# Performance work log

Hardware: AMD Instinct MI355X
Metric: run time of the kernel (lower is better)

The kernel has to match this reference:

```python
import jax, jax.numpy as jnp
import numpy as np

NEG_SLOPE = 0.01  # torch LeakyReLU default

def _rgcn_layer(x, comp_l, basis_l, root_l, bias_l, src, dst, etype, n_nodes):
    # basis decomposition: per-relation weight [R, in, out]
    w = jnp.einsum('rb,bio->rio', comp_l, basis_l)
    # transform every node by every relation: [N, R, out]
    xw = jnp.einsum('ni,rio->nro', x, w)
    # per-edge message = transformed source feature for the edge's relation
    m = xw[src, etype]                                  # [E, out]
    agg = jax.ops.segment_sum(m, dst, num_segments=n_nodes)  # scatter-add
    return agg + x @ root_l + bias_l

def setup_inputs() -> dict:
    key = jax.random.key(0)
    ks = jax.random.split(key, 12)
    N, E, R, B, D, L = 50000, 1600000, 8, 4, 240, 2
    s = 1.0 / np.sqrt(D)
    return {
        'x': jax.random.normal(ks[0], (N, D), jnp.float32),
        'edge_index': jax.random.randint(ks[1], (2, E), 0, N, jnp.int64),
        'edge_type': jax.random.randint(ks[2], (E,), 0, R, jnp.int64),
        'comp': jax.random.normal(ks[3], (L, R, B), jnp.float32) * 0.5,
        'basis': jax.random.normal(ks[4], (L, B, D, D), jnp.float32) * s,
        'root': jax.random.normal(ks[5], (L, D, D), jnp.float32) * s,
        'bias': jax.random.normal(ks[6], (L, D), jnp.float32) * 0.01,
        'W1': jax.random.normal(ks[7], (128, 2 * D), jnp.float32) / np.sqrt(2 * D),
        'b1': jax.random.normal(ks[8], (128,), jnp.float32) * 0.01,
        'W2': jax.random.normal(ks[9], (1, 128), jnp.float32) / np.sqrt(128),
        'b2': jax.random.normal(ks[10], (1,), jnp.float32) * 0.01,
        'concept_index': 0,
        'sentence_index': 1,
    }

def reference(x, edge_index, edge_type, comp, basis, root, bias, W1, b1, W2, b2,
              concept_index, sentence_index):
    n_nodes = x.shape[0]
    num_layers = comp.shape[0]
    src, dst = edge_index[0], edge_index[1]
    h = x
    for i in range(num_layers):
        h = _rgcn_layer(h, comp[i], basis[i], root[i], bias[i], src, dst, edge_type, n_nodes)
        if i != num_layers - 1:
            h = jax.nn.leaky_relu(h, NEG_SLOPE)  # dropout is identity at inference
    h_s = h[sentence_index]
    h_c = h[concept_index]
    h_cat = jnp.concatenate([jnp.abs(h_s - h_c), h_s * h_c], axis=-1)  # [2D]
    hidden = jax.nn.leaky_relu(h_cat @ W1.T + b1, NEG_SLOPE)
    out = hidden @ W2.T + b2  # [1]
    return out
```

## Files before the change

### kernel.cpp

```cpp
#include <hip/hip_runtime.h>
#include <cstdint>
#include <cstddef>

#define N_NODES 50000
#define N_EDGES 1600000
#define N_REL 8
#define N_BASIS 4
#define DIM 240
#define NEG_SLOPE 0.01f

#define CAP_S1 256
#define CAP_DEG 128
#define BITMAP_WORDS ((N_NODES + 31) / 32)
#define NCH 8
#define CHUNK (DIM / NCH)

__device__ __forceinline__ float lrelu(float v) { return v > 0.f ? v : NEG_SLOPE * v; }

__global__ __launch_bounds__(256) void k_pass1(const int* __restrict__ ei,
                                               const int* __restrict__ cip,
                                               const int* __restrict__ sip,
                                               unsigned* __restrict__ bitmap) {
    int base = (blockIdx.x * 256 + threadIdx.x) * 4;
    int ci = cip[0], si = sip[0];
    if (blockIdx.x == 0 && threadIdx.x == 0) {
        atomicOr(&bitmap[ci >> 5], 1u << (ci & 31));
        atomicOr(&bitmap[si >> 5], 1u << (si & 31));
    }
    if (base < N_EDGES) {
        int4 d = *reinterpret_cast<const int4*>(ei + N_EDGES + base);
        int dv[4] = {d.x, d.y, d.z, d.w};
#pragma unroll
        for (int j = 0; j < 4; j++) {
            if (dv[j] == ci || dv[j] == si) {
                int src = ei[base + j];
                atomicOr(&bitmap[src >> 5], 1u << (src & 31));
            }
        }
    }
}

__global__ __launch_bounds__(256) void k_compact(const unsigned* __restrict__ bitmap,
                                                 int* __restrict__ map,
                                                 int* __restrict__ nodes,
                                                 int* __restrict__ cnts) {
    int n = blockIdx.x * 256 + threadIdx.x;
    if (n < N_NODES && ((bitmap[n >> 5] >> (n & 31)) & 1u)) {
        int slot = atomicAdd(&cnts[0], 1);
        if (slot < CAP_S1) {
            map[n] = slot;
            nodes[slot] = n;
        } else {
            map[n] = -1;
        }
    }
}

__global__ __launch_bounds__(256) void k_pass2(const int* __restrict__ ei,
                                               const int* __restrict__ et,
                                               const unsigned* __restrict__ bitmap,
                                               const int* __restrict__ map,
                                               int* __restrict__ degs,
                                               unsigned* __restrict__ eslot) {
    int base = (blockIdx.x * 256 + threadIdx.x) * 4;
    if (base < N_EDGES) {
        int4 d = *reinterpret_cast<const int4*>(ei + N_EDGES + base);
        int dv[4] = {d.x, d.y, d.z, d.w};
#pragma unroll
        for (int j = 0; j < 4; j++) {
            int dst = dv[j];
            if ((bitmap[dst >> 5] >> (dst & 31)) & 1u) {
                int slot = map[dst];
                if (slot >= 0) {
                    int idx = atomicAdd(&degs[slot], 1);
                    if (idx < CAP_DEG) {
                        unsigned src = (unsigned)ei[base + j];
                        unsigned ty  = (unsigned)et[base + j];
                        eslot[(size_t)slot * CAP_DEG + idx] = src | (ty << 16);
                    }
                }
            }
        }
    }
}

__global__ __launch_bounds__(256) void k_z1(const float* __restrict__ x,
                                            const unsigned* __restrict__ eslot,
                                            const int* __restrict__ degs,
                                            const int* __restrict__ nodes,
                                            const int* __restrict__ cnts,
                                            const float* __restrict__ compL,
                                            float* __restrict__ z1) {
    int slot = blockIdx.x;
    if (slot >= min(cnts[0], CAP_S1)) return;
    int t = threadIdx.x;
    __shared__ unsigned els[CAP_DEG];
    __shared__ float cs[N_REL * N_BASIS];
    int deg = min(degs[slot], CAP_DEG);
    if (t < N_REL * N_BASIS) cs[t] = compL[t];
    if (t < deg) els[t] = eslot[(size_t)slot * CAP_DEG + t];
    __syncthreads();
    if (t < DIM) {
        float z0 = 0.f, z1a = 0.f, z2a = 0.f, z3a = 0.f;
        int base = 0;
        for (; base + 4 <= deg; base += 4) {
            float xv[4];
            int ty[4];
#pragma unroll
            for (int j = 0; j < 4; j++) {
                unsigned p = els[base + j];
                int src = (int)(p & 0xFFFFu);
                ty[j] = (int)(p >> 16);
                xv[j] = x[(size_t)src * DIM + t];
            }
#pragma unroll
            for (int j = 0; j < 4; j++) {
                const float* c = &cs[ty[j] * N_BASIS];
                z0 += c[0] * xv[j]; z1a += c[1] * xv[j];
                z2a += c[2] * xv[j]; z3a += c[3] * xv[j];
            }
        }
        for (; base < deg; base++) {
            unsigned p = els[base];
            int src = (int)(p & 0xFFFFu);
            const float* c = &cs[(p >> 16) * N_BASIS];
            float xv = x[(size_t)src * DIM + t];
            z0 += c[0] * xv; z1a += c[1] * xv; z2a += c[2] * xv; z3a += c[3] * xv;
        }
        int node = nodes[slot];
        float xn = x[(size_t)node * DIM + t];
        float* zp = z1 + (size_t)slot * 5 * DIM;
        zp[0 * DIM + t] = z0;  zp[1 * DIM + t] = z1a;
        zp[2 * DIM + t] = z2a; zp[3 * DIM + t] = z3a;
        zp[4 * DIM + t] = xn;
    }
}

__global__ __launch_bounds__(256) void k_hgemm(const float* __restrict__ z1,
                                               const int* __restrict__ cnts,
                                               const float* __restrict__ basisL,
                                               const float* __restrict__ rootL,
                                               float* __restrict__ h1raw) {
    int slot = blockIdx.x;
    if (slot >= min(cnts[0], CAP_S1)) return;
    int ch = blockIdx.y;
    int i0 = ch * CHUNK;
    int t = threadIdx.x;
    __shared__ float zc[5][CHUNK];
    if (t < 5 * CHUNK) {
        int b = t / CHUNK, ii = t % CHUNK;
        zc[b][ii] = z1[((size_t)slot * 5 + b) * DIM + i0 + ii];
    }
    __syncthreads();
    if (t < DIM) {
        float acc = 0.f;
#pragma unroll 5
        for (int ii = 0; ii < CHUNK; ii++) {
            int i = i0 + ii;
            acc += zc[0][ii] * basisL[(size_t)(0 * DIM + i) * DIM + t];
            acc += zc[1][ii] * basisL[(size_t)(1 * DIM + i) * DIM + t];
            acc += zc[2][ii] * basisL[(size_t)(2 * DIM + i) * DIM + t];
            acc += zc[3][ii] * basisL[(size_t)(3 * DIM + i) * DIM + t];
            acc += zc[4][ii] * rootL[(size_t)i * DIM + t];
        }
        atomicAdd(&h1raw[(size_t)slot * DIM + t], acc);
    }
}

__global__ __launch_bounds__(256) void k_zh2(const float* __restrict__ h1raw,
                                             const unsigned* __restrict__ eslot,
                                             const int* __restrict__ degs,
                                             const int* __restrict__ map,
                                             const float* __restrict__ comp2,
                                             const float* __restrict__ bias1,
                                             const float* __restrict__ basis2,
                                             const float* __restrict__ root2,
                                             const int* __restrict__ cip,
                                             const int* __restrict__ sip,
                                             float* __restrict__ h2acc) {
    int w = blockIdx.x, ch = blockIdx.y;
    int i0 = ch * CHUNK;
    int t = threadIdx.x;
    __shared__ unsigned els[CAP_DEG];
    __shared__ float cs[N_REL * N_BASIS];
    __shared__ float zpart[8][N_BASIS][CHUNK];
    __shared__ float zc[5][CHUNK];
    int node = w ? sip[0] : cip[0];
    int slot = map[node];
    int deg = (slot >= 0) ? min(degs[slot], CAP_DEG) : 0;
    if (t < N_REL * N_BASIS) cs[t] = comp2[t];
    if (t < deg) els[t] = eslot[(size_t)slot * CAP_DEG + t];
    __syncthreads();
    if (t < 8 * CHUNK) {
        int e8 = t / CHUNK, d = t % CHUNK;
        float za0 = 0.f, za1 = 0.f, za2 = 0.f, za3 = 0.f;
        for (int base = 0; base < deg; base += 8) {
            int e = base + e8;
            if (e < deg) {
                unsigned p = els[e];
                int src = (int)(p & 0xFFFFu);
                int ty  = (int)(p >> 16);
                int ss = map[src];
                float hv = 0.f;
                if (ss >= 0)
                    hv = lrelu(h1raw[(size_t)ss * DIM + i0 + d] + bias1[i0 + d]);
                const float* c = &cs[ty * N_BASIS];
                za0 += c[0] * hv; za1 += c[1] * hv; za2 += c[2] * hv; za3 += c[3] * hv;
            }
        }
        zpart[e8][0][d] = za0; zpart[e8][1][d] = za1;
        zpart[e8][2][d] = za2; zpart[e8][3][d] = za3;
    }
    __syncthreads();
    if (t < N_BASIS * CHUNK) {
        int b = t / CHUNK, d = t % CHUNK;
        float s = 0.f;
#pragma unroll
        for (int e = 0; e < 8; e++) s += zpart[e][b][d];
        zc[b][d] = s;
    } else if (t >= N_BASIS * CHUNK && t < 5 * CHUNK) {
        int d = t - N_BASIS * CHUNK;
        float r = (slot >= 0) ? lrelu(h1raw[(size_t)slot * DIM + i0 + d] + bias1[i0 + d]) : 0.f;
        zc[4][d] = r;
    }
    __syncthreads();
    if (t < DIM) {
        float acc = 0.f;
#pragma unroll 5
        for (int ii = 0; ii < CHUNK; ii++) {
            int i = i0 + ii;
            acc += zc[0][ii] * basis2[(size_t)(0 * DIM + i) * DIM + t];
            acc += zc[1][ii] * basis2[(size_t)(1 * DIM + i) * DIM + t];
            acc += zc[2][ii] * basis2[(size_t)(2 * DIM + i) * DIM + t];
            acc += zc[3][ii] * basis2[(size_t)(3 * DIM + i) * DIM + t];
            acc += zc[4][ii] * root2[(size_t)i * DIM + t];
        }
        atomicAdd(&h2acc[w * DIM + t], acc);
    }
}

__global__ __launch_bounds__(512) void k_head(const float* __restrict__ h2acc,
                                              const float* __restrict__ bias2,
                                              const float* __restrict__ W1,
                                              const float* __restrict__ b1,
                                              const float* __restrict__ W2,
                                              const float* __restrict__ b2,
                                              float* __restrict__ out) {
    __shared__ float cat[2 * DIM];
    __shared__ float part[128][4];
    __shared__ float hid[128];
    int t = threadIdx.x;
    if (t < DIM) {
        float hc = h2acc[t] + bias2[t];
        float hs = h2acc[DIM + t] + bias2[t];
        cat[t] = fabsf(hs - hc);
        cat[DIM + t] = hs * hc;
    }
    __syncthreads();
    int r = t >> 2, q = t & 3;
    const float4* wr = reinterpret_cast<const float4*>(W1 + (size_t)r * 2 * DIM) + q * 30;
    const float4* cq = reinterpret_cast<const float4*>(cat) + q * 30;
    float acc = 0.f;
#pragma unroll 6
    for (int k = 0; k < 30; k++) {
        float4 wv = wr[k];
        float4 cv = cq[k];
        acc += wv.x * cv.x + wv.y * cv.y + wv.z * cv.z + wv.w * cv.w;
    }
    part[r][q] = acc;
    __syncthreads();
    if (q == 0) {
        float s = part[r][0] + part[r][1] + part[r][2] + part[r][3] + b1[r];
        hid[r] = lrelu(s) * W2[r];
    }
    __syncthreads();
    if (t < 64) {
        float v = hid[t] + hid[t + 64];
        for (int off = 32; off > 0; off >>= 1) v += __shfl_down(v, off);
        if (t == 0) out[0] = b2[0] + v;
    }
}

extern "C" void kernel_launch(void* const* d_in, const int* in_sizes, int n_in,
                              void* d_out, int out_size, void* d_ws, size_t ws_size,
                              hipStream_t stream) {
    const float* x     = (const float*)d_in[0];
    const int*   ei    = (const int*)d_in[1];
    const int*   et    = (const int*)d_in[2];
    const float* comp  = (const float*)d_in[3];
    const float* basis = (const float*)d_in[4];
    const float* root  = (const float*)d_in[5];
    const float* bias  = (const float*)d_in[6];
    const float* W1    = (const float*)d_in[7];
    const float* b1    = (const float*)d_in[8];
    const float* W2    = (const float*)d_in[9];
    const float* b2    = (const float*)d_in[10];
    const int*   cip   = (const int*)d_in[11];
    const int*   sip   = (const int*)d_in[12];
    float* out = (float*)d_out;
    (void)n_in; (void)in_sizes; (void)out_size;

    char* ws = (char*)d_ws;
    size_t off = 0;
    auto alloc = [&](size_t bytes) -> char* {
        char* p = ws + off;
        off += (bytes + 255) & ~(size_t)255;
        return p;
    };
    size_t zbeg = off;
    int*      cnts   = (int*)alloc(2 * sizeof(int));
    int*      degs   = (int*)alloc((size_t)CAP_S1 * sizeof(int));
    unsigned* bitmap = (unsigned*)alloc(BITMAP_WORDS * sizeof(unsigned));
    float*    h2acc  = (float*)alloc((size_t)2 * DIM * sizeof(float));
    float*    h1raw  = (float*)alloc((size_t)CAP_S1 * DIM * sizeof(float));
    size_t zend = off;
    int*      map    = (int*)alloc((size_t)N_NODES * sizeof(int));
    int*      nodes  = (int*)alloc((size_t)CAP_S1 * sizeof(int));
    unsigned* eslot  = (unsigned*)alloc((size_t)CAP_S1 * CAP_DEG * sizeof(unsigned));
    float*    z1     = (float*)alloc((size_t)CAP_S1 * 5 * DIM * sizeof(float));
    if (off > ws_size) return;

    hipMemsetAsync(ws + zbeg, 0, zend - zbeg, stream);

    const float* comp2  = comp  + N_REL * N_BASIS;
    const float* basis2 = basis + (size_t)N_BASIS * DIM * DIM;
    const float* root2  = root  + (size_t)DIM * DIM;
    const float* bias2  = bias  + DIM;

    int egrid4 = (N_EDGES / 4 + 255) / 256;
    k_pass1<<<egrid4, 256, 0, stream>>>(ei, cip, sip, bitmap);
    k_compact<<<(N_NODES + 255) / 256, 256, 0, stream>>>(bitmap, map, nodes, cnts);
    k_pass2<<<egrid4, 256, 0, stream>>>(ei, et, bitmap, map, degs, eslot);

    k_z1<<<CAP_S1, 256, 0, stream>>>(x, eslot, degs, nodes, cnts, comp, z1);
    k_hgemm<<<dim3(CAP_S1, NCH), 256, 0, stream>>>(z1, cnts, basis, root, h1raw);
    k_zh2<<<dim3(2, NCH), 256, 0, stream>>>(h1raw, eslot, degs, map, comp2, bias,
                                            basis2, root2, cip, sip, h2acc);
    k_head<<<1, 512, 0, stream>>>(h2acc, bias2, W1, b1, W2, b2, out);
}
```

Measured before the change: 170.9 us.

## Fuse RGCN pipeline stages and drop bitmap/compact pass and memset

Replaces the bitmap, compact pass and memset with an init kernel plus atomicCAS claiming of node slots directly in the map. It fuses the per-node basis aggregation with the dense basis/root GEMM, recomputing the aggregation per output chunk instead of writing z1 and atomically adding partial results. The layer-2 stage and the MLP head are merged into one kernel, where the last block to finish (tracked by a completion counter) runs the head. This cuts the number of kernel launches and intermediate global traffic, at the cost of redundant gathers of x across the eight chunk blocks.

```diff
diff --git a/kernel.cpp b/kernel.cpp
--- a/kernel.cpp
+++ b/kernel.cpp
@@ -11,272 +11,265 @@
 
 #define CAP_S1 256
 #define CAP_DEG 128
-#define BITMAP_WORDS ((N_NODES + 31) / 32)
 #define NCH 8
 #define CHUNK (DIM / NCH)
 
+#define WS_CNT    0
+#define WS_DONE   8
+#define WS_DEGS   256
+#define WS_MAP    1280
+#define WS_NODES  201344
+#define WS_ESLOT  202496
+#define WS_H1C    333568
+#define WS_H2     579328
+#define WS_TOTAL  581248
+
 __device__ __forceinline__ float lrelu(float v) { return v > 0.f ? v : NEG_SLOPE * v; }
 
-__global__ __launch_bounds__(256) void k_pass1(const int* __restrict__ ei,
-                                               const int* __restrict__ cip,
-                                               const int* __restrict__ sip,
-                                               unsigned* __restrict__ bitmap) {
+__global__ __launch_bounds__(256) void k_init(int* __restrict__ cnt,
+                                              int* __restrict__ done,
+                                              int* __restrict__ degs,
+                                              int* __restrict__ map) {
+    int t = blockIdx.x * 256 + threadIdx.x;
+    int nth = gridDim.x * 256;
+    for (int n = t; n < N_NODES; n += nth) map[n] = -1;
+    for (int i = t; i < CAP_S1; i += nth) degs[i] = 0;
+    if (t == 0) { cnt[0] = 0; done[0] = 0; }
+}
+
+__device__ __forceinline__ void claim_node(int n, int* map, int* nodes, int* cnt) {
+    int old = atomicCAS(&map[n], -1, -2);
+    if (old == -1) {
+        int s = atomicAdd(cnt, 1);
+        if (s < CAP_S1) { nodes[s] = n; map[n] = s; }
+        else map[n] = -1;
+    }
+}
+
+__global__ __launch_bounds__(256) void k_mark(const int* __restrict__ ei,
+                                              const int* __restrict__ cip,
+                                              const int* __restrict__ sip,
+                                              int* __restrict__ map,
+                                              int* __restrict__ nodes,
+                                              int* __restrict__ cnt) {
     int base = (blockIdx.x * 256 + threadIdx.x) * 4;
     int ci = cip[0], si = sip[0];
-    if (blockIdx.x == 0 && threadIdx.x == 0) {
-        atomicOr(&bitmap[ci >> 5], 1u << (ci & 31));
-        atomicOr(&bitmap[si >> 5], 1u << (si & 31));
-    }
+    if (blockIdx.x == 0 && threadIdx.x < 2)
+        claim_node(threadIdx.x ? si : ci, map, nodes, cnt);
     if (base < N_EDGES) {
         int4 d = *reinterpret_cast<const int4*>(ei + N_EDGES + base);
         int dv[4] = {d.x, d.y, d.z, d.w};
 #pragma unroll
-        for (int j = 0; j < 4; j++) {
-            if (dv[j] == ci || dv[j] == si) {
-                int src = ei[base + j];
-                atomicOr(&bitmap[src >> 5], 1u << (src & 31));
-            }
-        }
-    }
-}
-
-__global__ __launch_bounds__(256) void k_compact(const unsigned* __restrict__ bitmap,
-                                                 int* __restrict__ map,
-                                                 int* __restrict__ nodes,
-                                                 int* __restrict__ cnts) {
-    int n = blockIdx.x * 256 + threadIdx.x;
-    if (n < N_NODES && ((bitmap[n >> 5] >> (n & 31)) & 1u)) {
-        int slot = atomicAdd(&cnts[0], 1);
-        if (slot < CAP_S1) {
-            map[n] = slot;
-            nodes[slot] = n;
-        } else {
-            map[n] = -1;
-        }
-    }
-}
-
-__global__ __launch_bounds__(256) void k_pass2(const int* __restrict__ ei,
-                                               const int* __restrict__ et,
-                                               const unsigned* __restrict__ bitmap,
-                                               const int* __restrict__ map,
-                                               int* __restrict__ degs,
-                                               unsigned* __restrict__ eslot) {
+        for (int j = 0; j < 4; j++)
+            if (dv[j] == ci || dv[j] == si)
+                claim_node(ei[base + j], map, nodes, cnt);
+    }
+}
+
+__global__ __launch_bounds__(256) void k_csr(const int* __restrict__ ei,
+                                             const int* __restrict__ et,
+                                             const int* __restrict__ map,
+                                             int* __restrict__ degs,
+                                             unsigned* __restrict__ eslot) {
     int base = (blockIdx.x * 256 + threadIdx.x) * 4;
     if (base < N_EDGES) {
         int4 d = *reinterpret_cast<const int4*>(ei + N_EDGES + base);
         int dv[4] = {d.x, d.y, d.z, d.w};
 #pragma unroll
         for (int j = 0; j < 4; j++) {
-            int dst = dv[j];
-            if ((bitmap[dst >> 5] >> (dst & 31)) & 1u) {
-                int slot = map[dst];
-                if (slot >= 0) {
-                    int idx = atomicAdd(&degs[slot], 1);
-                    if (idx < CAP_DEG) {
-                        unsigned src = (unsigned)ei[base + j];
-                        unsigned ty  = (unsigned)et[base + j];
-                        eslot[(size_t)slot * CAP_DEG + idx] = src | (ty << 16);
-                    }
-                }
+            int m = map[dv[j]];
+            if (m >= 0) {
+                int idx = atomicAdd(&degs[m], 1);
+                if (idx < CAP_DEG)
+                    eslot[(size_t)m * CAP_DEG + idx] =
+                        (unsigned)ei[base + j] | ((unsigned)et[base + j] << 16);
             }
         }
     }
 }
 
-__global__ __launch_bounds__(256) void k_z1(const float* __restrict__ x,
-                                            const unsigned* __restrict__ eslot,
-                                            const int* __restrict__ degs,
-                                            const int* __restrict__ nodes,
-                                            const int* __restrict__ cnts,
-                                            const float* __restrict__ compL,
-                                            float* __restrict__ z1) {
+__global__ __launch_bounds__(256) void k_zh1(const float* __restrict__ x,
+                                             const unsigned* __restrict__ eslot,
+                                             const int* __restrict__ degs,
+                                             const int* __restrict__ nodes,
+                                             const int* __restrict__ cnt,
+                                             const float* __restrict__ comp,
+                                             const float* __restrict__ basis,
+                                             const float* __restrict__ root,
+                                             const float* __restrict__ bias,
+                                             float* __restrict__ h1c) {
     int slot = blockIdx.x;
-    if (slot >= min(cnts[0], CAP_S1)) return;
+    if (slot >= min(cnt[0], CAP_S1)) return;
+    int j0 = blockIdx.y * CHUNK;
     int t = threadIdx.x;
+    __shared__ float zs[5][DIM];
     __shared__ unsigned els[CAP_DEG];
     __shared__ float cs[N_REL * N_BASIS];
+    __shared__ float red[NCH][CHUNK];
     int deg = min(degs[slot], CAP_DEG);
-    if (t < N_REL * N_BASIS) cs[t] = compL[t];
+    if (t < N_REL * N_BASIS) cs[t] = comp[t];
     if (t < deg) els[t] = eslot[(size_t)slot * CAP_DEG + t];
     __syncthreads();
     if (t < DIM) {
-        float z0 = 0.f, z1a = 0.f, z2a = 0.f, z3a = 0.f;
+        float a0 = 0.f, a1 = 0.f, a2 = 0.f, a3 = 0.f;
         int base = 0;
         for (; base + 4 <= deg; base += 4) {
-            float xv[4];
-            int ty[4];
+            float xv[4]; int ty[4];
 #pragma unroll
             for (int j = 0; j < 4; j++) {
                 unsigned p = els[base + j];
-                int src = (int)(p & 0xFFFFu);
                 ty[j] = (int)(p >> 16);
-                xv[j] = x[(size_t)src * DIM + t];
+                xv[j] = x[(size_t)(p & 0xFFFFu) * DIM + t];
             }
 #pragma unroll
             for (int j = 0; j < 4; j++) {
                 const float* c = &cs[ty[j] * N_BASIS];
-                z0 += c[0] * xv[j]; z1a += c[1] * xv[j];
-                z2a += c[2] * xv[j]; z3a += c[3] * xv[j];
+                a0 += c[0] * xv[j]; a1 += c[1] * xv[j];
+                a2 += c[2] * xv[j]; a3 += c[3] * xv[j];
             }
         }
         for (; base < deg; base++) {
             unsigned p = els[base];
-            int src = (int)(p & 0xFFFFu);
             const float* c = &cs[(p >> 16) * N_BASIS];
-            float xv = x[(size_t)src * DIM + t];
-            z0 += c[0] * xv; z1a += c[1] * xv; z2a += c[2] * xv; z3a += c[3] * xv;
-        }
-        int node = nodes[slot];
-        float xn = x[(size_t)node * DIM + t];
-        float* zp = z1 + (size_t)slot * 5 * DIM;
-        zp[0 * DIM + t] = z0;  zp[1 * DIM + t] = z1a;
-        zp[2 * DIM + t] = z2a; zp[3 * DIM + t] = z3a;
-        zp[4 * DIM + t] = xn;
-    }
-}
-
-__global__ __launch_bounds__(256) void k_hgemm(const float* __restrict__ z1,
-                                               const int* __restrict__ cnts,
-                                               const float* __restrict__ basisL,
-                                               const float* __restrict__ rootL,
-                                               float* __restrict__ h1raw) {
-    int slot = blockIdx.x;
-    if (slot >= min(cnts[0], CAP_S1)) return;
-    int ch = blockIdx.y;
-    int i0 = ch * CHUNK;
+            float xv = x[(size_t)(p & 0xFFFFu) * DIM + t];
+            a0 += c[0] * xv; a1 += c[1] * xv; a2 += c[2] * xv; a3 += c[3] * xv;
+        }
+        zs[0][t] = a0; zs[1][t] = a1; zs[2][t] = a2; zs[3][t] = a3;
+        zs[4][t] = x[(size_t)nodes[slot] * DIM + t];
+    }
+    __syncthreads();
+    if (t < DIM) {
+        int j = t % CHUNK, ip = t / CHUNK;
+        float acc = 0.f;
+#pragma unroll 6
+        for (int ii = 0; ii < CHUNK; ii++) {
+            int i = ip * CHUNK + ii;
+            int col = j0 + j;
+            acc += zs[0][i] * basis[(size_t)(0 * DIM + i) * DIM + col];
+            acc += zs[1][i] * basis[(size_t)(1 * DIM + i) * DIM + col];
+            acc += zs[2][i] * basis[(size_t)(2 * DIM + i) * DIM + col];
+            acc += zs[3][i] * basis[(size_t)(3 * DIM + i) * DIM + col];
+            acc += zs[4][i] * root[(size_t)i * DIM + col];
+        }
+        red[ip][j] = acc;
+    }
+    __syncthreads();
+    if (t < CHUNK) {
+        float s = 0.f;
+#pragma unroll
+        for (int ip = 0; ip < NCH; ip++) s += red[ip][t];
+        s += bias[j0 + t];
+        h1c[(size_t)slot * DIM + j0 + t] = lrelu(s);
+    }
+}
+
+__global__ __launch_bounds__(256) void k_zh2head(const float* __restrict__ h1c,
+                                                 const unsigned* __restrict__ eslot,
+                                                 const int* __restrict__ degs,
+                                                 const int* __restrict__ map,
+                                                 const float* __restrict__ comp2,
+                                                 const float* __restrict__ basis2,
+                                                 const float* __restrict__ root2,
+                                                 const float* __restrict__ bias2,
+                                                 const float* __restrict__ W1,
+                                                 const float* __restrict__ b1,
+                                                 const float* __restrict__ W2,
+                                                 const float* __restrict__ b2,
+                                                 const int* __restrict__ cip,
+                                                 const int* __restrict__ sip,
+                                                 float* __restrict__ h2,
+                                                 int* __restrict__ done,
+                                                 float* __restrict__ out) {
+    int bi = blockIdx.x;
+    int w = bi >> 3, j0 = (bi & 7) * CHUNK;
     int t = threadIdx.x;
-    __shared__ float zc[5][CHUNK];
-    if (t < 5 * CHUNK) {
-        int b = t / CHUNK, ii = t % CHUNK;
-        zc[b][ii] = z1[((size_t)slot * 5 + b) * DIM + i0 + ii];
-    }
-    __syncthreads();
-    if (t < DIM) {
-        float acc = 0.f;
-#pragma unroll 5
-        for (int ii = 0; ii < CHUNK; ii++) {
-            int i = i0 + ii;
-            acc += zc[0][ii] * basisL[(size_t)(0 * DIM + i) * DIM + t];
-            acc += zc[1][ii] * basisL[(size_t)(1 * DIM + i) * DIM + t];
-            acc += zc[2][ii] * basisL[(size_t)(2 * DIM + i) * DIM + t];
-            acc += zc[3][ii] * basisL[(size_t)(3 * DIM + i) * DIM + t];
-            acc += zc[4][ii] * rootL[(size_t)i * DIM + t];
-        }
-        atomicAdd(&h1raw[(size_t)slot * DIM + t], acc);
-    }
-}
-
-__global__ __launch_bounds__(256) void k_zh2(const float* __restrict__ h1raw,
-                                             const unsigned* __restrict__ eslot,
-                                             const int* __restrict__ degs,
-                                             const int* __restrict__ map,
-                                             const float* __restrict__ comp2,
-                                             const float* __restrict__ bias1,
-                                             const float* __restrict__ basis2,
-                                             const float* __restrict__ root2,
-                                             const int* __restrict__ cip,
-                                             const int* __restrict__ sip,
-                                             float* __restrict__ h2acc) {
-    int w = blockIdx.x, ch = blockIdx.y;
-    int i0 = ch * CHUNK;
-    int t = threadIdx.x;
+    __shared__ float zs[5][DIM];
     __shared__ unsigned els[CAP_DEG];
     __shared__ float cs[N_REL * N_BASIS];
-    __shared__ float zpart[8][N_BASIS][CHUNK];
-    __shared__ float zc[5][CHUNK];
+    __shared__ float red[NCH][CHUNK];
+    __shared__ int lastflag;
     int node = w ? sip[0] : cip[0];
     int slot = map[node];
     int deg = (slot >= 0) ? min(degs[slot], CAP_DEG) : 0;
     if (t < N_REL * N_BASIS) cs[t] = comp2[t];
     if (t < deg) els[t] = eslot[(size_t)slot * CAP_DEG + t];
     __syncthreads();
-    if (t < 8 * CHUNK) {
-        int e8 = t / CHUNK, d = t % CHUNK;
-        float za0 = 0.f, za1 = 0.f, za2 = 0.f, za3 = 0.f;
-        for (int base = 0; base < deg; base += 8) {
-            int e = base + e8;
-            if (e < deg) {
-                unsigned p = els[e];
-                int src = (int)(p & 0xFFFFu);
-                int ty  = (int)(p >> 16);
-                int ss = map[src];
-                float hv = 0.f;
-                if (ss >= 0)
-                    hv = lrelu(h1raw[(size_t)ss * DIM + i0 + d] + bias1[i0 + d]);
-                const float* c = &cs[ty * N_BASIS];
-                za0 += c[0] * hv; za1 += c[1] * hv; za2 += c[2] * hv; za3 += c[3] * hv;
+    if (t < DIM) {
+        float a0 = 0.f, a1 = 0.f, a2 = 0.f, a3 = 0.f;
+        for (int e = 0; e < deg; e++) {
+            unsigned p = els[e];
+            int ss = map[p & 0xFFFFu];
+            if (ss >= 0) {
+                float hv = h1c[(size_t)ss * DIM + t];
+                const float* c = &cs[(p >> 16) * N_BASIS];
+                a0 += c[0] * hv; a1 += c[1] * hv; a2 += c[2] * hv; a3 += c[3] * hv;
             }
         }
-        zpart[e8][0][d] = za0; zpart[e8][1][d] = za1;
-        zpart[e8][2][d] = za2; zpart[e8][3][d] = za3;
-    }
-    __syncthreads();
-    if (t < N_BASIS * CHUNK) {
-        int b = t / CHUNK, d = t % CHUNK;
+        zs[0][t] = a0; zs[1][t] = a1; zs[2][t] = a2; zs[3][t] = a3;
+        zs[4][t] = (slot >= 0) ? h1c[(size_t)slot * DIM + t] : 0.f;
+    }
+    __syncthreads();
+    if (t < DIM) {
+        int j = t % CHUNK, ip = t / CHUNK;
+        float acc = 0.f;
+#pragma unroll 6
+        for (int ii = 0; ii < CHUNK; ii++) {
+            int i = ip * CHUNK + ii;
+            int col = j0 + j;
+            acc += zs[0][i] * basis2[(size_t)(0 * DIM + i) * DIM + col];
+            acc += zs[1][i] * basis2[(size_t)(1 * DIM + i) * DIM + col];
+            acc += zs[2][i] * basis2[(size_t)(2 * DIM + i) * DIM + col];
+            acc += zs[3][i] * basis2[(size_t)(3 * DIM + i) * DIM + col];
+            acc += zs[4][i] * root2[(size_t)i * DIM + col];
+        }
+        red[ip][j] = acc;
+    }
+    __syncthreads();
+    if (t < CHUNK) {
         float s = 0.f;
 #pragma unroll
-        for (int e = 0; e < 8; e++) s += zpart[e][b][d];
-        zc[b][d] = s;
-    } else if (t >= N_BASIS * CHUNK && t < 5 * CHUNK) {
-        int d = t - N_BASIS * CHUNK;
-        float r = (slot >= 0) ? lrelu(h1raw[(size_t)slot * DIM + i0 + d] + bias1[i0 + d]) : 0.f;
-        zc[4][d] = r;
-    }
-    __syncthreads();
-    if (t < DIM) {
-        float acc = 0.f;
-#pragma unroll 5
-        for (int ii = 0; ii < CHUNK; ii++) {
-            int i = i0 + ii;
-            acc += zc[0][ii] * basis2[(size_t)(0 * DIM + i) * DIM + t];
-            acc += zc[1][ii] * basis2[(size_t)(1 * DIM + i) * DIM + t];
-            acc += zc[2][ii] * basis2[(size_t)(2 * DIM + i) * DIM + t];
-            acc += zc[3][ii] * basis2[(size_t)(3 * DIM + i) * DIM + t];
-            acc += zc[4][ii] * root2[(size_t)i * DIM + t];
-        }
-        atomicAdd(&h2acc[w * DIM + t], acc);
-    }
-}
-
-__global__ __launch_bounds__(512) void k_head(const float* __restrict__ h2acc,
-                                              const float* __restrict__ bias2,
-                                              const float* __restrict__ W1,
-                                              const float* __restrict__ b1,
-                                              const float* __restrict__ W2,
-                                              const float* __restrict__ b2,
-                                              float* __restrict__ out) {
+        for (int ip = 0; ip < NCH; ip++) s += red[ip][t];
+        h2[w * DIM + j0 + t] = s + bias2[j0 + t];
+    }
+    __threadfence();
+    __syncthreads();
+    if (t == 0) lastflag = (atomicAdd(done, 1) == 15) ? 1 : 0;
+    __syncthreads();
+    if (!lastflag) return;
+    __threadfence();
+
     __shared__ float cat[2 * DIM];
-    __shared__ float part[128][4];
+    __shared__ float part[128][2];
     __shared__ float hid[128];
-    int t = threadIdx.x;
-    if (t < DIM) {
-        float hc = h2acc[t] + bias2[t];
-        float hs = h2acc[DIM + t] + bias2[t];
+    if (t < DIM) {
+        float hc = h2[t];
+        float hs = h2[DIM + t];
         cat[t] = fabsf(hs - hc);
         cat[DIM + t] = hs * hc;
     }
     __syncthreads();
-    int r = t >> 2, q = t & 3;
-    const float4* wr = reinterpret_cast<const float4*>(W1 + (size_t)r * 2 * DIM) + q * 30;
-    const float4* cq = reinterpret_cast<const float4*>(cat) + q * 30;
-    float acc = 0.f;
+    {
+        int r = t >> 1, q = t & 1;
+        const float4* wr = reinterpret_cast<const float4*>(W1 + (size_t)r * 2 * DIM) + q * 60;
+        const float4* cq = reinterpret_cast<const float4*>(cat) + q * 60;
+        float acc = 0.f;
 #pragma unroll 6
-    for (int k = 0; k < 30; k++) {
-        float4 wv = wr[k];
-        float4 cv = cq[k];
-        acc += wv.x * cv.x + wv.y * cv.y + wv.z * cv.z + wv.w * cv.w;
-    }
-    part[r][q] = acc;
-    __syncthreads();
-    if (q == 0) {
-        float s = part[r][0] + part[r][1] + part[r][2] + part[r][3] + b1[r];
+        for (int k = 0; k < 60; k++) {
+            float4 wv = wr[k], cv = cq[k];
+            acc += wv.x * cv.x + wv.y * cv.y + wv.z * cv.z + wv.w * cv.w;
+        }
+        part[r][q] = acc;
+    }
+    __syncthreads();
+    if ((t & 1) == 0) {
+        int r = t >> 1;
+        float s = part[r][0] + part[r][1] + b1[r];
         hid[r] = lrelu(s) * W2[r];
     }
     __syncthreads();
     if (t < 64) {
         float v = hid[t] + hid[t + 64];
-        for (int off = 32; off > 0; off >>= 1) v += __shfl_down(v, off);
+        for (int o = 32; o > 0; o >>= 1) v += __shfl_down(v, o);
         if (t == 0) out[0] = b2[0] + v;
     }
 }
@@ -301,26 +294,16 @@
     (void)n_in; (void)in_sizes; (void)out_size;
 
     char* ws = (char*)d_ws;
-    size_t off = 0;
-    auto alloc = [&](size_t bytes) -> char* {
-        char* p = ws + off;
-        off += (bytes + 255) & ~(size_t)255;
-        return p;
-    };
-    size_t zbeg = off;
-    int*      cnts   = (int*)alloc(2 * sizeof(int));
-    int*      degs   = (int*)alloc((size_t)CAP_S1 * sizeof(int));
-    unsigned* bitmap = (unsigned*)alloc(BITMAP_WORDS * sizeof(unsigned));
-    float*    h2acc  = (float*)alloc((size_t)2 * DIM * sizeof(float));
-    float*    h1raw  = (float*)alloc((size_t)CAP_S1 * DIM * sizeof(float));
-    size_t zend = off;
-    int*      map    = (int*)alloc((size_t)N_NODES * sizeof(int));
-    int*      nodes  = (int*)alloc((size_t)CAP_S1 * sizeof(int));
-    unsigned* eslot  = (unsigned*)alloc((size_t)CAP_S1 * CAP_DEG * sizeof(unsigned));
-    float*    z1     = (float*)alloc((size_t)CAP_S1 * 5 * DIM * sizeof(float));
-    if (off > ws_size) return;
-
-    hipMemsetAsync(ws + zbeg, 0, zend - zbeg, stream);
+    if (ws_size < WS_TOTAL) return;
+
+    int*      cnt   = (int*)(ws + WS_CNT);
+    int*      done  = (int*)(ws + WS_DONE);
+    int*      degs  = (int*)(ws + WS_DEGS);
+    int*      map   = (int*)(ws + WS_MAP);
+    int*      nodes = (int*)(ws + WS_NODES);
+    unsigned* eslot = (unsigned*)(ws + WS_ESLOT);
+    float*    h1c   = (float*)(ws + WS_H1C);
+    float*    h2    = (float*)(ws + WS_H2);
 
     const float* comp2  = comp  + N_REL * N_BASIS;
     const float* basis2 = basis + (size_t)N_BASIS * DIM * DIM;
@@ -328,13 +311,12 @@
     const float* bias2  = bias  + DIM;
 
     int egrid4 = (N_EDGES / 4 + 255) / 256;
-    k_pass1<<<egrid4, 256, 0, stream>>>(ei, cip, sip, bitmap);
-    k_compact<<<(N_NODES + 255) / 256, 256, 0, stream>>>(bitmap, map, nodes, cnts);
-    k_pass2<<<egrid4, 256, 0, stream>>>(ei, et, bitmap, map, degs, eslot);
-
-    k_z1<<<CAP_S1, 256, 0, stream>>>(x, eslot, degs, nodes, cnts, comp, z1);
-    k_hgemm<<<dim3(CAP_S1, NCH), 256, 0, stream>>>(z1, cnts, basis, root, h1raw);
-    k_zh2<<<dim3(2, NCH), 256, 0, stream>>>(h1raw, eslot, degs, map, comp2, bias,
-                                            basis2, root2, cip, sip, h2acc);
-    k_head<<<1, 512, 0, stream>>>(h2acc, bias2, W1, b1, W2, b2, out);
-}
+
+    k_init<<<256, 256, 0, stream>>>(cnt, done, degs, map);
+    k_mark<<<egrid4, 256, 0, stream>>>(ei, cip, sip, map, nodes, cnt);
+    k_csr<<<egrid4, 256, 0, stream>>>(ei, et, map, degs, eslot);
+    k_zh1<<<dim3(CAP_S1, NCH), 256, 0, stream>>>(x, eslot, degs, nodes, cnt,
+                                                 comp, basis, root, bias, h1c);
+    k_zh2head<<<16, 256, 0, stream>>>(h1c, eslot, degs, map, comp2, basis2, root2,
+                                      bias2, W1, b1, W2, b2, cip, sip, h2, done, out);
+}
```

New measurement: 168.4 us. No clear change (-1.5%).
